# Optimization experiments

Measured on AMD Instinct MI355X. Metric: run time of the kernel, lower is better.

The kernel has to match this reference:

```python
import jax, jax.numpy as jnp
from jax import lax
import numpy as np

B, CIN, H, S = 32, 16, 64, 128
TAU = 0.5


def _conv1d(x, w, b, dilation):
    # x: [B, C, S], w: [O, I, K] -> [B, O, S], stride 1, SAME padding (matches torch padding='same')
    y = lax.conv_general_dilated(x, w, window_strides=(1,), padding='SAME',
                                 rhs_dilation=(dilation,),
                                 dimension_numbers=('NCH', 'OIH', 'NCH'))
    return y + b[None, :, None]


def setup_inputs() -> dict:
    key = jax.random.key(0)
    ks = jax.random.split(key, 16)
    def w(k, shape, fan_in):
        return jax.random.normal(k, shape, jnp.float32) * (1.0 / np.sqrt(fan_in))
    inp = {
        'data': jax.random.normal(ks[0], (B, 1, CIN, S), jnp.float32),
        'conv11_w': w(ks[1], (H, CIN, 1), CIN), 'conv11_b': jnp.zeros((H,), jnp.float32),
        'conv12_w': w(ks[2], (H, H, 3), H * 3), 'conv12_b': jnp.zeros((H,), jnp.float32),
        'conv21_w': w(ks[3], (H, CIN, 1), CIN), 'conv21_b': jnp.zeros((H,), jnp.float32),
        'conv22_w': w(ks[4], (H, H, 5), H * 5), 'conv22_b': jnp.zeros((H,), jnp.float32),
        'conv31_w': w(ks[5], (H, CIN, 5), CIN * 5), 'conv31_b': jnp.zeros((H,), jnp.float32),
        'fc_final_w': w(ks[6], (H, 3 * H), 3 * H), 'fc_final_b': jnp.zeros((H,), jnp.float32),
        'fc1_w': w(ks[7], (H, 2 * H), 2 * H), 'fc1_b': jnp.zeros((H,), jnp.float32),
        'fc2_w': w(ks[8], (2, H), H), 'fc2_b': jnp.zeros((2,), jnp.float32),
        # pre-sampled uniform noise for gumbel-softmax (deterministic reference)
        'gumbel_u': jax.random.uniform(ks[9], (B, S * S, 2), jnp.float32, 1e-7, 1.0 - 1e-7),
    }
    return inp


def reference(data, conv11_w, conv11_b, conv12_w, conv12_b, conv21_w, conv21_b,
              conv22_w, conv22_b, conv31_w, conv31_b, fc_final_w, fc_final_b,
              fc1_w, fc1_b, fc2_w, fc2_b, gumbel_u):
    x = data[:, 0].astype(jnp.float32)                      # [B, CIN, S]
    x1 = _conv1d(_conv1d(x, conv11_w, conv11_b, 1), conv12_w, conv12_b, 3)
    x2 = _conv1d(_conv1d(x, conv21_w, conv21_b, 1), conv22_w, conv22_b, 5)
    x3 = _conv1d(x, conv31_w, conv31_b, 1)
    h = jnp.concatenate([x1, x2, x3], axis=1)               # [B, 3H, S]
    h = jnp.swapaxes(h, 1, 2)                               # [B, S, 3H]
    h = jax.nn.relu(h @ fc_final_w.T + fc_final_b)          # [B, S, H]

    # one-hot matmuls are exact gathers: rec rows = repeat, send cols = tile
    rows = jnp.repeat(jnp.arange(S), S)                     # [S*S]
    cols = jnp.tile(jnp.arange(S), S)                       # [S*S]
    receivers = h[:, rows]                                  # [B, S*S, H]
    senders = h[:, cols]                                    # [B, S*S, H]
    e = jnp.concatenate([senders, receivers], axis=2)       # [B, S*S, 2H]
    e = jax.nn.relu(e @ fc1_w.T + fc1_b)
    logits = e @ fc2_w.T + fc2_b                            # [B, S*S, 2]

    # gumbel-softmax, hard=True (straight-through)
    g = -jnp.log(-jnp.log(gumbel_u))
    y_soft = jax.nn.softmax((logits + g) / TAU, axis=-1)
    y_hard = jax.nn.one_hot(jnp.argmax(y_soft, axis=-1), 2, dtype=y_soft.dtype)
    y = lax.stop_gradient(y_hard - y_soft) + y_soft

    a = y[..., 0].reshape(-1, S, S)                         # [B, S, S]
    keep = jnp.triu(jnp.ones((S, S), bool), k=1)            # zero lower tri and diagonal
    return jnp.where(keep, a, jnp.zeros((), a.dtype))
```

## Files before the change

### kernel.cpp

```cpp
#include <hip/hip_runtime.h>
#include <math.h>

#define BB   32
#define CIN  16
#define HH   64
#define SS   128


__global__ __launch_bounds__(256) void prep1(
    const float* __restrict__ w11, const float* __restrict__ w21,
    const float* __restrict__ w12, const float* __restrict__ w22,
    const float* __restrict__ b11, const float* __restrict__ b21,
    const float* __restrict__ b12, const float* __restrict__ b22,
    const float* __restrict__ wf,
    double* __restrict__ W1e, double* __restrict__ W2e,
    double* __restrict__ wfT, double* __restrict__ b1e,
    double* __restrict__ b2e)
{
    int o = blockIdx.x * 256 + threadIdx.x;
    if (o < 3072) {
        int m = o / 48, r = o % 48, c = r / 3, t = r % 3;
        double a0 = 0, a1 = 0;
        #pragma unroll
        for (int mm = 0; mm < 64; mm += 2) {
            a0 += (double)w12[(m*64+mm)*3+t]   * (double)w11[mm*16+c];
            a1 += (double)w12[(m*64+mm+1)*3+t] * (double)w11[(mm+1)*16+c];
        }
        W1e[o] = a0 + a1;
    } else if (o < 8192) {
        int j = o - 3072;
        int m = j / 80, r = j % 80, c = r / 5, u = r % 5;
        double a0 = 0, a1 = 0;
        #pragma unroll
        for (int mm = 0; mm < 64; mm += 2) {
            a0 += (double)w22[(m*64+mm)*5+u]   * (double)w21[mm*16+c];
            a1 += (double)w22[(m*64+mm+1)*5+u] * (double)w21[(mm+1)*16+c];
        }
        W2e[j] = a0 + a1;
    } else if (o < 20480) {
        int j = o - 8192;
        wfT[j] = (double)wf[(j & 63) * 192 + (j >> 6)];
    } else if (o < 28672) {
        int j = o - 20480; int m = j >> 7, p = j & 127;
        double a = (double)b12[m];
        #pragma unroll
        for (int t = 0; t < 3; ++t) {
            int pos = p + (t - 1) * 3;
            if (pos >= 0 && pos < SS) {
                double s0 = 0, s1 = 0;
                #pragma unroll
                for (int mm = 0; mm < 64; mm += 2) {
                    s0 += (double)w12[(m*64+mm)*3+t]   * (double)b11[mm];
                    s1 += (double)w12[(m*64+mm+1)*3+t] * (double)b11[mm+1];
                }
                a += s0 + s1;
            }
        }
        b1e[j] = a;
    } else if (o < 36864) {
        int j = o - 28672; int m = j >> 7, p = j & 127;
        double a = (double)b22[m];
        #pragma unroll
        for (int u = 0; u < 5; ++u) {
            int pos = p + (u - 2) * 5;
            if (pos >= 0 && pos < SS) {
                double s0 = 0, s1 = 0;
                #pragma unroll
                for (int mm = 0; mm < 64; mm += 2) {
                    s0 += (double)w22[(m*64+mm)*5+u]   * (double)b21[mm];
                    s1 += (double)w22[(m*64+mm+1)*5+u] * (double)b21[mm+1];
                }
                a += s0 + s1;
            }
        }
        b2e[j] = a;
    }
}

__global__ __launch_bounds__(256) void prep2(
    const float* __restrict__ bf,  const float* __restrict__ b31,
    const float* __restrict__ w31,
    const double* __restrict__ W1e, const double* __restrict__ W2e,
    const double* __restrict__ wfT, const double* __restrict__ b1e,
    const double* __restrict__ b2e,
    double* __restrict__ T, double* __restrict__ Be)
{
    int o = blockIdx.x * 256 + threadIdx.x;
    if (o < 11264) {
        int n = o & 63, k = o >> 6, c = k / 11, ti = k % 11;
        double a0 = 0, a1 = 0;
        if (ti == 2 || ti == 5 || ti == 8) {
            int t = (ti - 2) / 3;
            #pragma unroll
            for (int m = 0; m < 64; m += 2) {
                a0 += wfT[m*64+n]     * W1e[m*48 + c*3 + t];
                a1 += wfT[(m+1)*64+n] * W1e[(m+1)*48 + c*3 + t];
            }
        }
        if (ti == 0 || ti == 1 || ti == 5 || ti == 9 || ti == 10) {
            int u = (ti == 0) ? 0 : (ti == 1) ? 1 : (ti == 5) ? 2 : (ti == 9) ? 3 : 4;
            #pragma unroll
            for (int m = 0; m < 64; m += 2) {
                a0 += wfT[(64+m)*64+n]   * W2e[m*80 + c*5 + u];
                a1 += wfT[(64+m+1)*64+n] * W2e[(m+1)*80 + c*5 + u];
            }
        }
        if (ti >= 3 && ti <= 7) {
            int v = ti - 3;
            #pragma unroll
            for (int m = 0; m < 64; m += 2) {
                a0 += wfT[(128+m)*64+n]   * (double)w31[(m*16+c)*5+v];
                a1 += wfT[(128+m+1)*64+n] * (double)w31[((m+1)*16+c)*5+v];
            }
        }
        T[k*64+n] = a0 + a1;
    } else if (o < 19456) {
        int j = o - 11264; int n = j & 63, p = j >> 6;
        double a0 = (double)bf[n], a1 = 0, a2 = 0;
        #pragma unroll
        for (int m = 0; m < 64; ++m) {
            a0 += wfT[m*64+n]       * b1e[m*128+p];
            a1 += wfT[(64+m)*64+n]  * b2e[m*128+p];
            a2 += wfT[(128+m)*64+n] * (double)b31[m];
        }
        Be[p*64+n] = a0 + a1 + a2;
    }
}

__global__ __launch_bounds__(512, 1) void front(
    const float* __restrict__ x,   const double* __restrict__ T,
    const double* __restrict__ Be, const float* __restrict__ w1,
    const float* __restrict__ b1,
    double* __restrict__ Qg, double* __restrict__ Pg)
{
    const int b  = blockIdx.y;
    const int s0 = blockIdx.x * 16;
    const int t  = threadIdx.x;
    const int lane = t & 63, wave = t >> 6;
    const int kq = wave & 3, ph = wave >> 2;

    __shared__ float  xl[CIN][37];
    __shared__ float  E[176 * 16];
    __shared__ float  w1L[128 * 65];
    __shared__ double red [4][16][64];
    __shared__ double redP[4][16][64];
    __shared__ double h[64 * 18];
    __shared__ int    COL[11];

    double wT[44];
    #pragma unroll
    for (int kk = 0; kk < 44; ++kk) wT[kk] = T[(kq*44+kk)*64 + lane];

    if (t < 11) { const int offs[11] = {-10,-5,-3,-2,-1,0,1,2,3,5,10}; COL[t] = offs[t] + 10; }
    for (int e = t; e < CIN * 36; e += 512) {
        int c = e / 36, col = e - c * 36;
        int g = s0 - 10 + col;
        xl[c][col] = (g >= 0 && g < SS) ? x[(b * CIN + c) * SS + g] : 0.f;
    }
    for (int e = t; e < 8192; e += 512) {
        int n = e >> 7, k = e & 127;
        w1L[k * 65 + n] = w1[e];
    }
    __syncthreads();
    for (int e = t; e < 2816; e += 512) {
        int k = e >> 4, p = e & 15;
        int c = k / 11, ti = k - c * 11;
        E[e] = xl[c][p + COL[ti]];
    }
    __syncthreads();

    double acc[8];
    #pragma unroll
    for (int q = 0; q < 8; ++q) acc[q] = 0.0;
    #pragma unroll
    for (int kk = 0; kk < 44; ++kk) {
        const float4* dp = (const float4*)(E + (kq*44+kk)*16 + ph*8);
        float4 v0 = dp[0], v1 = dp[1];
        double w = wT[kk];
        acc[0] += (double)v0.x * w; acc[1] += (double)v0.y * w;
        acc[2] += (double)v0.z * w; acc[3] += (double)v0.w * w;
        acc[4] += (double)v1.x * w; acc[5] += (double)v1.y * w;
        acc[6] += (double)v1.z * w; acc[7] += (double)v1.w * w;
    }
    if (kq) { for (int q = 0; q < 8; ++q) red[kq][ph*8+q][lane] = acc[q]; }
    __syncthreads();
    if (!kq) {
        for (int q = 0; q < 8; ++q) {
            int p = ph*8 + q;
            double tot = acc[q] + red[1][p][lane] + red[2][p][lane] + red[3][p][lane]
                       + Be[(s0 + p) * 64 + lane];
            h[lane*18 + p] = tot > 0.0 ? tot : 0.0;
        }
    }
    __syncthreads();

    double aq[8], ap[8];
    #pragma unroll
    for (int q = 0; q < 8; ++q) { aq[q] = 0.0; ap[q] = 0.0; }
    #pragma unroll
    for (int kk = 0; kk < 16; ++kk) {
        int k = kq*16 + kk;
        double q_ = (double)w1L[k * 65 + lane];
        double p_ = (double)w1L[(64 + k) * 65 + lane];
        const double2* hp = (const double2*)(h + k*18 + ph*8);
        double2 d0 = hp[0], d1 = hp[1], d2 = hp[2], d3 = hp[3];
        aq[0] += d0.x*q_; ap[0] += d0.x*p_;  aq[1] += d0.y*q_; ap[1] += d0.y*p_;
        aq[2] += d1.x*q_; ap[2] += d1.x*p_;  aq[3] += d1.y*q_; ap[3] += d1.y*p_;
        aq[4] += d2.x*q_; ap[4] += d2.x*p_;  aq[5] += d2.y*q_; ap[5] += d2.y*p_;
        aq[6] += d3.x*q_; ap[6] += d3.x*p_;  aq[7] += d3.y*q_; ap[7] += d3.y*p_;
    }
    if (kq) {
        for (int q = 0; q < 8; ++q) {
            red [kq][ph*8+q][lane] = aq[q];
            redP[kq][ph*8+q][lane] = ap[q];
        }
    }
    __syncthreads();
    if (!kq) {
        double bv = (double)b1[lane];
        for (int q = 0; q < 8; ++q) {
            int p = ph*8 + q;
            Qg[((long)b*SS + s0 + p)*HH + lane] =
                aq[q] + red[1][p][lane] + red[2][p][lane] + red[3][p][lane];
            Pg[((long)b*SS + s0 + p)*HH + lane] =
                ap[q] + redP[1][p][lane] + redP[2][p][lane] + redP[3][p][lane] + bv;
        }
    }
}

__global__ __launch_bounds__(256) void edges(
    const double* __restrict__ Qg, const double* __restrict__ Pg,
    const float* __restrict__ w2, const float* __restrict__ b2,
    const float* __restrict__ gum, float* __restrict__ out)
{
    const int b  = blockIdx.y;
    const int it = blockIdx.x >> 2;
    const int jt = blockIdx.x & 3;
    const int i0 = it * 16, j0 = jt * 32;
    const int t  = threadIdx.x;
    const int ti = t >> 4, tj = t & 15;
    const int i  = i0 + ti;

    if (j0 + 31 < i0) {
        out[((long)b*SS + i)*SS + j0 + tj]      = 0.f;
        out[((long)b*SS + i)*SS + j0 + tj + 16] = 0.f;
        return;
    }

    __shared__ float Pl[16][68];
    __shared__ float Ql[32][68];
    __shared__ float dwl[64];

    if (t < 64) dwl[t] = w2[t] - w2[64 + t];
    for (int e = t; e < 1024; e += 256) {
        int r = e >> 6, c = e & 63;
        Pl[r][c] = (float)Pg[((long)b*SS + i0 + r)*HH + c];
    }
    for (int e = t; e < 2048; e += 256) {
        int r = e >> 6, c = e & 63;
        Ql[r][c] = (float)Qg[((long)b*SS + j0 + r)*HH + c];
    }
    __syncthreads();

    float a0 = 0.f, a1 = 0.f;
    const float4* P0 = (const float4*)&Pl[ti][0];
    const float4* Q0 = (const float4*)&Ql[tj][0];
    const float4* Q1 = (const float4*)&Ql[tj + 16][0];
    const float4* DW = (const float4*)dwl;
#define RDOT(acc, pv, qv, dw) { float v; \
    v = pv.x + qv.x; v = v > 0.f ? v : 0.f; acc += v * dw.x; \
    v = pv.y + qv.y; v = v > 0.f ? v : 0.f; acc += v * dw.y; \
    v = pv.z + qv.z; v = v > 0.f ? v : 0.f; acc += v * dw.z; \
    v = pv.w + qv.w; v = v > 0.f ? v : 0.f; acc += v * dw.w; }
    #pragma unroll
    for (int k4 = 0; k4 < 16; ++k4) {
        float4 pv = P0[k4], dw = DW[k4];
        float4 q0 = Q0[k4], q1 = Q1[k4];
        RDOT(a0, pv, q0, dw)
        RDOT(a1, pv, q1, dw)
    }
#undef RDOT
    const float db2 = b2[0] - b2[1];
    float accs[2] = {a0, a1};
    for (int jj = 0; jj < 2; ++jj) {
        int j = j0 + tj + 16*jj;
        float r = 0.f;
        if (j > i) {
            long e = (long)b*SS*SS + (long)i*SS + j;
            float2 uv = *(const float2*)(gum + e*2);
            float tot = db2 - logf(-logf(uv.x)) + logf(-logf(uv.y)) + accs[jj];
            if (fabsf(tot) < 1e-4f) {
                const double* Prd = Pg + ((long)b*SS + i)*HH;
                const double* Qrd = Qg + ((long)b*SS + j)*HH;
                double s0=0, s1=0, s2=0, s3=0;
                #pragma unroll
                for (int k = 0; k < 64; k += 4) {
                    double v0 = Prd[k]   + Qrd[k];
                    double v1 = Prd[k+1] + Qrd[k+1];
                    double v2 = Prd[k+2] + Qrd[k+2];
                    double v3 = Prd[k+3] + Qrd[k+3];
                    if (v0 > 0.0) s0 += v0 * ((double)w2[k]   - (double)w2[64+k]);
                    if (v1 > 0.0) s1 += v1 * ((double)w2[k+1] - (double)w2[64+k+1]);
                    if (v2 > 0.0) s2 += v2 * ((double)w2[k+2] - (double)w2[64+k+2]);
                    if (v3 > 0.0) s3 += v3 * ((double)w2[k+3] - (double)w2[64+k+3]);
                }
                double accd = (double)b2[0] - (double)b2[1]
                            - log(-log((double)uv.x)) + log(-log((double)uv.y))
                            + ((s0 + s1) + (s2 + s3));
                r = (accd >= 0.0) ? 1.0f : 0.0f;
            } else {
                r = (tot >= 0.f) ? 1.0f : 0.0f;
            }
        }
        out[((long)b*SS + i)*SS + j] = r;
    }
}

extern "C" void kernel_launch(void* const* d_in, const int* in_sizes, int n_in,
                              void* d_out, int out_size, void* d_ws, size_t ws_size,
                              hipStream_t stream) {
    const float* data = (const float*)d_in[0];
    const float* w11  = (const float*)d_in[1];
    const float* b11  = (const float*)d_in[2];
    const float* w12  = (const float*)d_in[3];
    const float* b12  = (const float*)d_in[4];
    const float* w21  = (const float*)d_in[5];
    const float* b21  = (const float*)d_in[6];
    const float* w22  = (const float*)d_in[7];
    const float* b22  = (const float*)d_in[8];
    const float* w31  = (const float*)d_in[9];
    const float* b31  = (const float*)d_in[10];
    const float* wf   = (const float*)d_in[11];
    const float* bf   = (const float*)d_in[12];
    const float* w1   = (const float*)d_in[13];
    const float* b1   = (const float*)d_in[14];
    const float* w2   = (const float*)d_in[15];
    const float* b2   = (const float*)d_in[16];
    const float* gum  = (const float*)d_in[17];
    float* out = (float*)d_out;

    double* T   = (double*)d_ws;
    double* Be  = T   + 11264;
    double* Qg  = Be  + 8192;
    double* Pg  = Qg  + 262144;
    double* W1e = Qg;
    double* W2e = W1e + 3072;
    double* wfT = W2e + 5120;
    double* b1e = wfT + 12288;
    double* b2e = b1e + 8192;

    prep1<<<144, 256, 0, stream>>>(w11, w21, w12, w22, b11, b21, b12, b22, wf,
                                   W1e, W2e, wfT, b1e, b2e);
    prep2<<<76, 256, 0, stream>>>(bf, b31, w31, W1e, W2e, wfT, b1e, b2e, T, Be);
    front<<<dim3(8, BB), 512, 0, stream>>>(data, T, Be, w1, b1, Qg, Pg);
    edges<<<dim3(32, BB), 256, 0, stream>>>(Qg, Pg, w2, b2, gum, out);
}
```

Measured before the change: 55.07 us.

## Merge weight-folding prep kernels into one and vectorize edge loads

Merges the two weight-precomputation kernels into a single kernel. Each block loads the fc_final weight into shared memory and computes the folded conv weights it needs locally, so the global double-precision intermediates (W1e, W2e, wfT, b1e, b2e) are no longer written and read back. The bias folding is rewritten as per-tap partial sums plus boundary masks instead of a per-position recompute. The edges kernel now loads P and Q rows as double2 pairs. This removes one launch and a global round-trip, but every prep block redundantly stages the full 192x64 weight into shared memory.

```diff
diff --git a/kernel.cpp b/kernel.cpp
--- a/kernel.cpp
+++ b/kernel.cpp
@@ -7,123 +7,128 @@
 #define SS   128
 
 
-__global__ __launch_bounds__(256) void prep1(
+__global__ __launch_bounds__(256) void prep(
     const float* __restrict__ w11, const float* __restrict__ w21,
     const float* __restrict__ w12, const float* __restrict__ w22,
+    const float* __restrict__ w31, const float* __restrict__ wf,
+    const float* __restrict__ bf,
     const float* __restrict__ b11, const float* __restrict__ b21,
     const float* __restrict__ b12, const float* __restrict__ b22,
-    const float* __restrict__ wf,
-    double* __restrict__ W1e, double* __restrict__ W2e,
-    double* __restrict__ wfT, double* __restrict__ b1e,
-    double* __restrict__ b2e)
+    const float* __restrict__ b31,
+    double* __restrict__ T, double* __restrict__ Be)
 {
-    int o = blockIdx.x * 256 + threadIdx.x;
-    if (o < 3072) {
-        int m = o / 48, r = o % 48, c = r / 3, t = r % 3;
+    __shared__ float  wfl[192 * 65];
+    __shared__ double W1s[4][64];
+    __shared__ double W2s[4][64];
+    __shared__ double SW1s[64][3];
+    __shared__ double SW2s[64][5];
+
+    const int tid = threadIdx.x;
+    const int bx  = blockIdx.x;
+
+    for (int e = tid; e < 12288; e += 256) {
+        int n = e / 192, m = e - n * 192;
+        wfl[m * 65 + n] = wf[e];
+    }
+
+    if (bx < 44) {
+        const int slot = tid >> 6, n = tid & 63;
+        const int k = bx * 4 + slot, c = k / 11, ti = k % 11;
+        const bool p1 = (ti == 2 || ti == 5 || ti == 8);
+        const bool p2 = (ti == 0 || ti == 1 || ti == 5 || ti == 9 || ti == 10);
+        const bool p3 = (ti >= 3 && ti <= 7);
+        if (p1) {
+            int t = (ti - 2) / 3;
+            double s0 = 0, s1 = 0;
+            #pragma unroll
+            for (int mm = 0; mm < 64; mm += 2) {
+                s0 += (double)w12[(n*64+mm)*3+t]   * (double)w11[mm*16+c];
+                s1 += (double)w12[(n*64+mm+1)*3+t] * (double)w11[(mm+1)*16+c];
+            }
+            W1s[slot][n] = s0 + s1;
+        }
+        if (p2) {
+            int u = (ti == 0) ? 0 : (ti == 1) ? 1 : (ti == 5) ? 2 : (ti == 9) ? 3 : 4;
+            double s0 = 0, s1 = 0;
+            #pragma unroll
+            for (int mm = 0; mm < 64; mm += 2) {
+                s0 += (double)w22[(n*64+mm)*5+u]   * (double)w21[mm*16+c];
+                s1 += (double)w22[(n*64+mm+1)*5+u] * (double)w21[(mm+1)*16+c];
+            }
+            W2s[slot][n] = s0 + s1;
+        }
+        __syncthreads();
         double a0 = 0, a1 = 0;
-        #pragma unroll
-        for (int mm = 0; mm < 64; mm += 2) {
-            a0 += (double)w12[(m*64+mm)*3+t]   * (double)w11[mm*16+c];
-            a1 += (double)w12[(m*64+mm+1)*3+t] * (double)w11[(mm+1)*16+c];
-        }
-        W1e[o] = a0 + a1;
-    } else if (o < 8192) {
-        int j = o - 3072;
-        int m = j / 80, r = j % 80, c = r / 5, u = r % 5;
-        double a0 = 0, a1 = 0;
-        #pragma unroll
-        for (int mm = 0; mm < 64; mm += 2) {
-            a0 += (double)w22[(m*64+mm)*5+u]   * (double)w21[mm*16+c];
-            a1 += (double)w22[(m*64+mm+1)*5+u] * (double)w21[(mm+1)*16+c];
-        }
-        W2e[j] = a0 + a1;
-    } else if (o < 20480) {
-        int j = o - 8192;
-        wfT[j] = (double)wf[(j & 63) * 192 + (j >> 6)];
-    } else if (o < 28672) {
-        int j = o - 20480; int m = j >> 7, p = j & 127;
-        double a = (double)b12[m];
-        #pragma unroll
-        for (int t = 0; t < 3; ++t) {
-            int pos = p + (t - 1) * 3;
-            if (pos >= 0 && pos < SS) {
+        if (p1) {
+            #pragma unroll
+            for (int m = 0; m < 64; m += 2) {
+                a0 += (double)wfl[m*65+n]     * W1s[slot][m];
+                a1 += (double)wfl[(m+1)*65+n] * W1s[slot][m+1];
+            }
+        }
+        if (p2) {
+            #pragma unroll
+            for (int m = 0; m < 64; m += 2) {
+                a0 += (double)wfl[(64+m)*65+n]   * W2s[slot][m];
+                a1 += (double)wfl[(64+m+1)*65+n] * W2s[slot][m+1];
+            }
+        }
+        if (p3) {
+            int v = ti - 3;
+            #pragma unroll
+            for (int m = 0; m < 64; m += 2) {
+                a0 += (double)wfl[(128+m)*65+n]   * (double)w31[(m*16+c)*5+v];
+                a1 += (double)wfl[(128+m+1)*65+n] * (double)w31[((m+1)*16+c)*5+v];
+            }
+        }
+        T[k * 64 + n] = a0 + a1;
+    } else {
+        for (int q = tid; q < 512; q += 256) {
+            if (q < 192) {
+                int m = q / 3, t = q - 3 * m;
                 double s0 = 0, s1 = 0;
                 #pragma unroll
                 for (int mm = 0; mm < 64; mm += 2) {
                     s0 += (double)w12[(m*64+mm)*3+t]   * (double)b11[mm];
                     s1 += (double)w12[(m*64+mm+1)*3+t] * (double)b11[mm+1];
                 }
-                a += s0 + s1;
-            }
-        }
-        b1e[j] = a;
-    } else if (o < 36864) {
-        int j = o - 28672; int m = j >> 7, p = j & 127;
-        double a = (double)b22[m];
-        #pragma unroll
-        for (int u = 0; u < 5; ++u) {
-            int pos = p + (u - 2) * 5;
-            if (pos >= 0 && pos < SS) {
+                SW1s[m][t] = s0 + s1;
+            } else {
+                int q2 = q - 192; int m = q2 / 5, u = q2 - 5 * m;
                 double s0 = 0, s1 = 0;
                 #pragma unroll
                 for (int mm = 0; mm < 64; mm += 2) {
                     s0 += (double)w22[(m*64+mm)*5+u]   * (double)b21[mm];
                     s1 += (double)w22[(m*64+mm+1)*5+u] * (double)b21[mm+1];
                 }
-                a += s0 + s1;
-            }
-        }
-        b2e[j] = a;
-    }
-}
-
-__global__ __launch_bounds__(256) void prep2(
-    const float* __restrict__ bf,  const float* __restrict__ b31,
-    const float* __restrict__ w31,
-    const double* __restrict__ W1e, const double* __restrict__ W2e,
-    const double* __restrict__ wfT, const double* __restrict__ b1e,
-    const double* __restrict__ b2e,
-    double* __restrict__ T, double* __restrict__ Be)
-{
-    int o = blockIdx.x * 256 + threadIdx.x;
-    if (o < 11264) {
-        int n = o & 63, k = o >> 6, c = k / 11, ti = k % 11;
-        double a0 = 0, a1 = 0;
-        if (ti == 2 || ti == 5 || ti == 8) {
-            int t = (ti - 2) / 3;
-            #pragma unroll
-            for (int m = 0; m < 64; m += 2) {
-                a0 += wfT[m*64+n]     * W1e[m*48 + c*3 + t];
-                a1 += wfT[(m+1)*64+n] * W1e[(m+1)*48 + c*3 + t];
-            }
-        }
-        if (ti == 0 || ti == 1 || ti == 5 || ti == 9 || ti == 10) {
-            int u = (ti == 0) ? 0 : (ti == 1) ? 1 : (ti == 5) ? 2 : (ti == 9) ? 3 : 4;
-            #pragma unroll
-            for (int m = 0; m < 64; m += 2) {
-                a0 += wfT[(64+m)*64+n]   * W2e[m*80 + c*5 + u];
-                a1 += wfT[(64+m+1)*64+n] * W2e[(m+1)*80 + c*5 + u];
-            }
-        }
-        if (ti >= 3 && ti <= 7) {
-            int v = ti - 3;
-            #pragma unroll
-            for (int m = 0; m < 64; m += 2) {
-                a0 += wfT[(128+m)*64+n]   * (double)w31[(m*16+c)*5+v];
-                a1 += wfT[(128+m+1)*64+n] * (double)w31[((m+1)*16+c)*5+v];
-            }
-        }
-        T[k*64+n] = a0 + a1;
-    } else if (o < 19456) {
-        int j = o - 11264; int n = j & 63, p = j >> 6;
-        double a0 = (double)bf[n], a1 = 0, a2 = 0;
+                SW2s[m][u] = s0 + s1;
+            }
+        }
+        __syncthreads();
+        int j = (bx - 44) * 256 + tid;
+        int n = tid & 63, p = j >> 6;
+        double base = (double)bf[n];
+        double d10 = 0, d12 = 0, d20 = 0, d21 = 0, d23 = 0, d24 = 0;
         #pragma unroll
         for (int m = 0; m < 64; ++m) {
-            a0 += wfT[m*64+n]       * b1e[m*128+p];
-            a1 += wfT[(64+m)*64+n]  * b2e[m*128+p];
-            a2 += wfT[(128+m)*64+n] * (double)b31[m];
-        }
-        Be[p*64+n] = a0 + a1 + a2;
+            double wa = (double)wfl[m*65+n];
+            double wb = (double)wfl[(64+m)*65+n];
+            double wc = (double)wfl[(128+m)*65+n];
+            base += wa * ((double)b12[m] + SW1s[m][1])
+                  + wb * ((double)b22[m] + SW2s[m][2])
+                  + wc * (double)b31[m];
+            d10 += wa * SW1s[m][0];  d12 += wa * SW1s[m][2];
+            d20 += wb * SW2s[m][0];  d21 += wb * SW2s[m][1];
+            d23 += wb * SW2s[m][3];  d24 += wb * SW2s[m][4];
+        }
+        double a = base;
+        if (p >= 3)   a += d10;
+        if (p <= 124) a += d12;
+        if (p >= 10)  a += d20;
+        if (p >= 5)   a += d21;
+        if (p <= 122) a += d23;
+        if (p <= 117) a += d24;
+        Be[p * 64 + n] = a;
     }
 }
 
@@ -252,13 +257,15 @@
     __shared__ float dwl[64];
 
     if (t < 64) dwl[t] = w2[t] - w2[64 + t];
+    for (int e = t; e < 512; e += 256) {
+        int r = e >> 5, c2 = (e & 31) * 2;
+        double2 v = *(const double2*)(Pg + ((long)b*SS + i0 + r)*HH + c2);
+        Pl[r][c2] = (float)v.x; Pl[r][c2+1] = (float)v.y;
+    }
     for (int e = t; e < 1024; e += 256) {
-        int r = e >> 6, c = e & 63;
-        Pl[r][c] = (float)Pg[((long)b*SS + i0 + r)*HH + c];
-    }
-    for (int e = t; e < 2048; e += 256) {
-        int r = e >> 6, c = e & 63;
-        Ql[r][c] = (float)Qg[((long)b*SS + j0 + r)*HH + c];
+        int r = e >> 5, c2 = (e & 31) * 2;
+        double2 v = *(const double2*)(Qg + ((long)b*SS + j0 + r)*HH + c2);
+        Ql[r][c2] = (float)v.x; Ql[r][c2+1] = (float)v.y;
     }
     __syncthreads();
 
@@ -339,19 +346,13 @@
     const float* gum  = (const float*)d_in[17];
     float* out = (float*)d_out;
 
-    double* T   = (double*)d_ws;
-    double* Be  = T   + 11264;
-    double* Qg  = Be  + 8192;
-    double* Pg  = Qg  + 262144;
-    double* W1e = Qg;
-    double* W2e = W1e + 3072;
-    double* wfT = W2e + 5120;
-    double* b1e = wfT + 12288;
-    double* b2e = b1e + 8192;
-
-    prep1<<<144, 256, 0, stream>>>(w11, w21, w12, w22, b11, b21, b12, b22, wf,
-                                   W1e, W2e, wfT, b1e, b2e);
-    prep2<<<76, 256, 0, stream>>>(bf, b31, w31, W1e, W2e, wfT, b1e, b2e, T, Be);
+    double* T  = (double*)d_ws;
+    double* Be = T  + 11264;
+    double* Qg = Be + 8192;
+    double* Pg = Qg + 262144;
+
+    prep<<<76, 256, 0, stream>>>(w11, w21, w12, w22, w31, wf, bf,
+                                 b11, b21, b12, b22, b31, T, Be);
     front<<<dim3(8, BB), 512, 0, stream>>>(data, T, Be, w1, b1, Qg, Pg);
     edges<<<dim3(32, BB), 256, 0, stream>>>(Qg, Pg, w2, b2, gum, out);
 }
```

After: 50.40 us. 1.09x faster.
